# Kernel tuning notes

Measured on AMD Instinct MI355X. Metric: run time of the kernel, lower is better.

## Reference

```python
import jax, jax.numpy as jnp
import numpy as np

E, B, D, F, H, L = 100, 4096, 256, 32, 16, 8  # estimators, batch, input_dim, max_features, F/2, latent


def setup_inputs() -> dict:
    key = jax.random.key(0)
    ks = jax.random.split(key, 16)
    s = 0.1
    return {
        "x": jax.random.normal(ks[0], (B, D), jnp.float32),
        "idx": jax.random.randint(ks[1], (E, F), 0, D),
        "We0": jax.random.normal(ks[2], (E, F, H), jnp.float32) * s,
        "be0": jax.random.normal(ks[3], (E, H), jnp.float32) * s,
        "We1": jax.random.normal(ks[4], (E, H, L), jnp.float32) * s,
        "be1": jax.random.normal(ks[5], (E, L), jnp.float32) * s,
        "Wl": jax.random.normal(ks[6], (E, L, L), jnp.float32) * s,
        "bl": jax.random.normal(ks[7], (E, L), jnp.float32) * s,
        "Wd0": jax.random.normal(ks[8], (E, L, H), jnp.float32) * s,
        "bd0": jax.random.normal(ks[9], (E, H), jnp.float32) * s,
        "Wd1": jax.random.normal(ks[10], (E, H, F), jnp.float32) * s,
        "bd1": jax.random.normal(ks[11], (E, F), jnp.float32) * s,
        "Wo": jax.random.normal(ks[12], (E, F, D), jnp.float32) * s,
        "bo": jax.random.normal(ks[13], (E, D), jnp.float32) * s,
    }


def reference(x, idx, We0, be0, We1, be1, Wl, bl, Wd0, bd0, Wd1, bd1, Wo, bo):
    # Gather per-estimator feature subsets: x[:, idx] -> [B, E, F] -> [E, B, F]
    xg = jnp.transpose(x[:, idx], (1, 0, 2))
    # Encoder: hidden[0] (no ReLU, matches original), hidden[1] + ReLU, latent + ReLU
    h0 = jnp.einsum('ebf,efh->ebh', xg, We0) + be0[:, None, :]
    h1 = jax.nn.relu(jnp.einsum('ebh,ehl->ebl', h0, We1) + be1[:, None, :])
    z = jax.nn.relu(jnp.einsum('ebl,elm->ebm', h1, Wl) + bl[:, None, :])
    # Decoder: hidden[0] (no ReLU), hidden[1] + ReLU, out + sigmoid
    d0 = jnp.einsum('ebl,elh->ebh', z, Wd0) + bd0[:, None, :]
    d1 = jax.nn.relu(jnp.einsum('ebh,ehf->ebf', d0, Wd1) + bd1[:, None, :])
    o = jax.nn.sigmoid(jnp.einsum('ebf,efd->ebd', d1, Wo) + bo[:, None, :])
    return o  # [E, B, D]
```

## Files before the change

### kernel.cpp

```cpp
#include <hip/hip_runtime.h>
#include <hip/hip_bf16.h>

#define NE 100
#define NB 4096
#define ND 256
#define NF 32
#define NH 16
#define NL 8
#define BT 256
#define S_REP 264

typedef float    floatx4 __attribute__((ext_vector_type(4)));
typedef _Float16 half8   __attribute__((ext_vector_type(8)));

#define NLOG2E -1.44269504088896f

__device__ __forceinline__ float sig2(float a) {
    return __builtin_amdgcn_rcpf(1.0f + __builtin_amdgcn_exp2f(a));
}

__global__ __launch_bounds__(256, 2)
void bagae_mfma(const float* __restrict__ x,
                const int* __restrict__ idx,
                const float* __restrict__ We0, const float* __restrict__ be0,
                const float* __restrict__ We1, const float* __restrict__ be1,
                const float* __restrict__ Wl,  const float* __restrict__ bl,
                const float* __restrict__ Wd0, const float* __restrict__ bd0,
                const float* __restrict__ Wd1, const float* __restrict__ bd1,
                const float* __restrict__ Wo,  const float* __restrict__ bo,
                float* __restrict__ out)
{
    __shared__ float sPool[4 * 16 * S_REP];
    __shared__ float s_We0[NF * NH];
    __shared__ float s_We1[NH * NL];
    __shared__ float s_Wl [NL * NL];
    __shared__ float s_Wd0[NL * NH];
    __shared__ float s_Wd1[NH * NF];
    __shared__ float s_be0[NH], s_be1[NL], s_bl[NL], s_bd0[NH], s_bd1[NF];
    __shared__ int   s_idx[NF];

    _Float16* sA = reinterpret_cast<_Float16*>(sPool);
    _Float16* sB = reinterpret_cast<_Float16*>(sPool) + BT * NF;

    const int tid = threadIdx.x;
    const int e   = blockIdx.y;
    const int b0  = blockIdx.x * BT;

    {
        const float* We0e = We0 + e * (NF * NH);
        const float* Wd1e = Wd1 + e * (NH * NF);
        for (int i = tid; i < NF * NH; i += 256) { s_We0[i] = We0e[i]; s_Wd1[i] = Wd1e[i]; }
        if (tid < NH * NL) { s_We1[tid] = We1[e * NH * NL + tid];
                             s_Wd0[tid] = Wd0[e * NL * NH + tid]; }
        if (tid < NL * NL) { s_Wl[tid]  = Wl [e * NL * NL + tid]; }
        if (tid < NF)      { s_idx[tid] = idx[e * NF + tid];
                             s_bd1[tid] = bd1[e * NF + tid]; }
        if (tid < NH)      { s_be0[tid] = be0[e * NH + tid];
                             s_bd0[tid] = bd0[e * NH + tid]; }
        if (tid < NL)      { s_be1[tid] = be1[e * NL + tid];
                             s_bl [tid] = bl [e * NL + tid]; }
    }

    {
        const float* Woe = Wo + (long)e * NF * ND;
        float wcol[NF];
        #pragma unroll
        for (int k = 0; k < NF; ++k) wcol[k] = Woe[k * ND + tid];
        const int ct = tid >> 4, c16 = tid & 15;
        #pragma unroll
        for (int kc = 0; kc < 4; ++kc) {
            half8 v;
            #pragma unroll
            for (int j = 0; j < 8; ++j) v[j] = (_Float16)(wcol[kc * 8 + j] * NLOG2E);
            const int u = (ct * 4 + kc) * 16 + c16;
            *reinterpret_cast<half8*>(&sB[u * 8]) = v;
        }
    }
    __syncthreads();

    {
        const float* xrow = x + (long)(b0 + tid) * ND;

        float xg[NF];
        #pragma unroll
        for (int f = 0; f < NF; ++f) xg[f] = xrow[s_idx[f]];

        float h0[NH];
        #pragma unroll
        for (int h = 0; h < NH; ++h) h0[h] = s_be0[h];
        #pragma unroll
        for (int f = 0; f < NF; ++f) {
            #pragma unroll
            for (int h = 0; h < NH; ++h)
                h0[h] = fmaf(xg[f], s_We0[f * NH + h], h0[h]);
        }

        float h1[NL];
        #pragma unroll
        for (int l = 0; l < NL; ++l) h1[l] = s_be1[l];
        #pragma unroll
        for (int h = 0; h < NH; ++h) {
            #pragma unroll
            for (int l = 0; l < NL; ++l)
                h1[l] = fmaf(h0[h], s_We1[h * NL + l], h1[l]);
        }
        #pragma unroll
        for (int l = 0; l < NL; ++l) h1[l] = fmaxf(h1[l], 0.0f);

        float zz[NL];
        #pragma unroll
        for (int m = 0; m < NL; ++m) zz[m] = s_bl[m];
        #pragma unroll
        for (int l = 0; l < NL; ++l) {
            #pragma unroll
            for (int m = 0; m < NL; ++m)
                zz[m] = fmaf(h1[l], s_Wl[l * NL + m], zz[m]);
        }
        #pragma unroll
        for (int m = 0; m < NL; ++m) zz[m] = fmaxf(zz[m], 0.0f);

        float d0[NH];
        #pragma unroll
        for (int h = 0; h < NH; ++h) d0[h] = s_bd0[h];
        #pragma unroll
        for (int l = 0; l < NL; ++l) {
            #pragma unroll
            for (int h = 0; h < NH; ++h)
                d0[h] = fmaf(zz[l], s_Wd0[l * NH + h], d0[h]);
        }

        float d1[NF];
        #pragma unroll
        for (int f = 0; f < NF; ++f) d1[f] = s_bd1[f];
        #pragma unroll
        for (int h = 0; h < NH; ++h) {
            #pragma unroll
            for (int f = 0; f < NF; ++f)
                d1[f] = fmaf(d0[h], s_Wd1[h * NF + f], d1[f]);
        }

        const int t = tid >> 4, r16 = tid & 15;
        #pragma unroll
        for (int kc = 0; kc < 4; ++kc) {
            half8 v;
            #pragma unroll
            for (int j = 0; j < 8; ++j)
                v[j] = (_Float16)fmaxf(d1[kc * 8 + j], 0.0f);
            const int u = (t * 4 + kc) * 16 + r16;
            *reinterpret_cast<half8*>(&sA[u * 8]) = v;
        }
    }
    __syncthreads();

    const int w   = tid >> 6;
    const int l   = tid & 63;
    const int r16 = l & 15;
    const int cq  = (l >> 4) * 4;

    half8 bfr[16];
    #pragma unroll
    for (int ct = 0; ct < 16; ++ct)
        bfr[ct] = *reinterpret_cast<const half8*>(&sB[(ct * 64 + l) * 8]);
    half8 afr[4];
    #pragma unroll
    for (int i = 0; i < 4; ++i)
        afr[i] = *reinterpret_cast<const half8*>(&sA[((w * 4 + i) * 64 + l) * 8]);

    __syncthreads();

    {
        float* rep = &sPool[w * 16 * S_REP];

        #pragma unroll
        for (int i = 0; i < 4; ++i) {
            const int rt = w * 4 + i;

            #pragma unroll
            for (int ct = 0; ct < 16; ++ct) {
                floatx4 b4 = *reinterpret_cast<const floatx4*>(bo + e * ND + ct * 16 + cq);
                floatx4 acc = b4 * NLOG2E;
                acc = __builtin_amdgcn_mfma_f32_16x16x32_f16(bfr[ct], afr[i], acc, 0, 0, 0);
                floatx4 o;
                o.x = sig2(acc[0]);
                o.y = sig2(acc[1]);
                o.z = sig2(acc[2]);
                o.w = sig2(acc[3]);
                *reinterpret_cast<floatx4*>(&rep[r16 * S_REP + ct * 16 + cq]) = o;
            }

            float* obase = out + ((long)e * NB + b0 + rt * 16) * ND + 4 * l;
            #pragma unroll
            for (int r = 0; r < 16; ++r) {
                floatx4 v = *reinterpret_cast<const floatx4*>(&rep[r * S_REP + 4 * l]);
                __builtin_nontemporal_store(v, reinterpret_cast<floatx4*>(obase + (long)r * ND));
            }
        }
    }
}

extern "C" void kernel_launch(void* const* d_in, const int* in_sizes, int n_in,
                              void* d_out, int out_size, void* d_ws, size_t ws_size,
                              hipStream_t stream) {
    const float* x   = (const float*)d_in[0];
    const int*   idx = (const int*)  d_in[1];
    const float* We0 = (const float*)d_in[2];
    const float* be0 = (const float*)d_in[3];
    const float* We1 = (const float*)d_in[4];
    const float* be1 = (const float*)d_in[5];
    const float* Wl  = (const float*)d_in[6];
    const float* bl  = (const float*)d_in[7];
    const float* Wd0 = (const float*)d_in[8];
    const float* bd0 = (const float*)d_in[9];
    const float* Wd1 = (const float*)d_in[10];
    const float* bd1 = (const float*)d_in[11];
    const float* Wo  = (const float*)d_in[12];
    const float* bo  = (const float*)d_in[13];
    float* out = (float*)d_out;

    dim3 grid(NB / BT, NE);
    dim3 block(256);
    hipLaunchKernelGGL(bagae_mfma, grid, block, 0, stream,
                       x, idx, We0, be0, We1, be1, Wl, bl,
                       Wd0, bd0, Wd1, bd1, Wo, bo, out);
}
```

Baseline: 118.2 us.

## Software-pipeline output tile stores with next tile's MFMA and sigmoid

```diff
diff --git a/kernel.cpp b/kernel.cpp
--- a/kernel.cpp
+++ b/kernel.cpp
@@ -31,6 +31,7 @@
                 float* __restrict__ out)
 {
     __shared__ float sPool[4 * 16 * S_REP];
+    __shared__ float sBias[ND];
     __shared__ float s_We0[NF * NH];
     __shared__ float s_We1[NH * NL];
     __shared__ float s_Wl [NL * NL];
@@ -50,6 +51,7 @@
         const float* We0e = We0 + e * (NF * NH);
         const float* Wd1e = Wd1 + e * (NH * NF);
         for (int i = tid; i < NF * NH; i += 256) { s_We0[i] = We0e[i]; s_Wd1[i] = Wd1e[i]; }
+        sBias[tid] = bo[e * ND + tid] * NLOG2E;
         if (tid < NH * NL) { s_We1[tid] = We1[e * NH * NL + tid];
                              s_Wd0[tid] = Wd0[e * NL * NH + tid]; }
         if (tid < NL * NL) { s_Wl[tid]  = Wl [e * NL * NL + tid]; }
@@ -170,31 +172,48 @@
 
     {
         float* rep = &sPool[w * 16 * S_REP];
-
-        #pragma unroll
-        for (int i = 0; i < 4; ++i) {
-            const int rt = w * 4 + i;
-
-            #pragma unroll
-            for (int ct = 0; ct < 16; ++ct) {
-                floatx4 b4 = *reinterpret_cast<const floatx4*>(bo + e * ND + ct * 16 + cq);
-                floatx4 acc = b4 * NLOG2E;
-                acc = __builtin_amdgcn_mfma_f32_16x16x32_f16(bfr[ct], afr[i], acc, 0, 0, 0);
-                floatx4 o;
-                o.x = sig2(acc[0]);
-                o.y = sig2(acc[1]);
-                o.z = sig2(acc[2]);
-                o.w = sig2(acc[3]);
-                *reinterpret_cast<floatx4*>(&rep[r16 * S_REP + ct * 16 + cq]) = o;
+        const long orow0 = (long)e * NB + b0 + w * 64;
+
+        #define COMPUTE_CT(i_, ct_)                                                     \
+        {                                                                               \
+            floatx4 acc = *reinterpret_cast<const floatx4*>(&sBias[(ct_) * 16 + cq]);   \
+            acc = __builtin_amdgcn_mfma_f32_16x16x32_f16(bfr[(ct_)], afr[(i_)], acc, 0, 0, 0); \
+            floatx4 o;                                                                  \
+            o.x = sig2(acc[0]);                                                         \
+            o.y = sig2(acc[1]);                                                         \
+            o.z = sig2(acc[2]);                                                         \
+            o.w = sig2(acc[3]);                                                         \
+            *reinterpret_cast<floatx4*>(&rep[r16 * S_REP + (ct_) * 16 + cq]) = o;       \
+        }
+
+        #pragma unroll
+        for (int ct = 0; ct < 16; ++ct) COMPUTE_CT(0, ct)
+        floatx4 rows[16];
+        #pragma unroll
+        for (int r = 0; r < 16; ++r)
+            rows[r] = *reinterpret_cast<const floatx4*>(&rep[r * S_REP + 4 * l]);
+
+        #pragma unroll
+        for (int i = 1; i < 4; ++i) {
+            float* obase = out + (orow0 + (long)(i - 1) * 16) * ND + 4 * l;
+            #pragma unroll
+            for (int r = 0; r < 16; ++r) {
+                __builtin_nontemporal_store(rows[r],
+                    reinterpret_cast<floatx4*>(obase + (long)r * ND));
+                COMPUTE_CT(i, r)
             }
-
-            float* obase = out + ((long)e * NB + b0 + rt * 16) * ND + 4 * l;
-            #pragma unroll
-            for (int r = 0; r < 16; ++r) {
-                floatx4 v = *reinterpret_cast<const floatx4*>(&rep[r * S_REP + 4 * l]);
-                __builtin_nontemporal_store(v, reinterpret_cast<floatx4*>(obase + (long)r * ND));
-            }
-        }
+            #pragma unroll
+            for (int r = 0; r < 16; ++r)
+                rows[r] = *reinterpret_cast<const floatx4*>(&rep[r * S_REP + 4 * l]);
+        }
+        {
+            float* obase = out + (orow0 + 48) * ND + 4 * l;
+            #pragma unroll
+            for (int r = 0; r < 16; ++r)
+                __builtin_nontemporal_store(rows[r],
+                    reinterpret_cast<floatx4*>(obase + (long)r * ND));
+        }
+        #undef COMPUTE_CT
     }
 }
 
```

Result: faster. 115.5 us (-2.2%).
